# Kernel tuning notes

Hardware: AMD Instinct MI355X
Metric: run time of the kernel (lower is better)

Reference implementation:

```python
import jax, jax.numpy as jnp
import numpy as np
from functools import partial

L, E, H, FF = 6, 768, 12, 3072
D = E // H
EPS = 1e-5

def _layernorm(x, g, b):
    mu = jnp.mean(x, axis=-1, keepdims=True)
    var = jnp.mean(jnp.square(x - mu), axis=-1, keepdims=True)
    return (x - mu) * jax.lax.rsqrt(var + EPS) * g + b

def setup_inputs() -> dict:
    key = jax.random.key(0)
    ks = jax.random.split(key, 16)
    s = 0.02
    return {
        "inputs_embeds": jax.random.normal(ks[0], (2, 1024, E), jnp.float32),
        "attention_mask": jnp.ones((2, 1024), jnp.float32),
        "Wqkv": jax.random.normal(ks[1], (L, E, 3 * E), jnp.float32) * s,
        "bqkv": jnp.zeros((L, 3 * E), jnp.float32),
        "Wo": jax.random.normal(ks[2], (L, E, E), jnp.float32) * s,
        "bo": jnp.zeros((L, E), jnp.float32),
        "ln1_g": jnp.ones((L, E), jnp.float32),
        "ln1_b": jnp.zeros((L, E), jnp.float32),
        "ln2_g": jnp.ones((L, E), jnp.float32),
        "ln2_b": jnp.zeros((L, E), jnp.float32),
        "Wfc": jax.random.normal(ks[3], (L, E, FF), jnp.float32) * s,
        "bfc": jnp.zeros((L, FF), jnp.float32),
        "Wmo": jax.random.normal(ks[4], (L, FF, E), jnp.float32) * s,
        "bmo": jnp.zeros((L, E), jnp.float32),
        "lnf_g": jnp.ones((E,), jnp.float32),
        "lnf_b": jnp.zeros((E,), jnp.float32),
    }

def reference(inputs_embeds, attention_mask, Wqkv, bqkv, Wo, bo,
              ln1_g, ln1_b, ln2_g, ln2_b, Wfc, bfc, Wmo, bmo, lnf_g, lnf_b):
    B, S, _ = inputs_embeds.shape
    # additive mask, broadcast over heads and query positions: [B,1,1,S]
    mask_add = (1.0 - attention_mask)[:, None, None, :] * -10000.0
    scale = 1.0 / jnp.sqrt(jnp.float32(D))

    def block(x, p):
        wqkv, bq, wo_, bo_, g1, b1, g2, b2, wfc, bf, wmo, bm = p
        h = _layernorm(x, g1, b1)
        qkv = h @ wqkv + bq                      # [B,S,3E]
        q, k, v = jnp.split(qkv, 3, axis=-1)
        q = q.reshape(B, S, H, D).transpose(0, 2, 1, 3)  # [B,H,S,D]
        k = k.reshape(B, S, H, D).transpose(0, 2, 1, 3)
        v = v.reshape(B, S, H, D).transpose(0, 2, 1, 3)
        scores = jnp.einsum('bhqd,bhkd->bhqk', q, k) * scale + mask_add
        w = jax.nn.softmax(scores, axis=-1)
        a = jnp.einsum('bhqk,bhkd->bhqd', w, v)
        a = a.transpose(0, 2, 1, 3).reshape(B, S, E)
        x = x + a @ wo_ + bo_
        m = _layernorm(x, g2, b2)
        m = jax.nn.gelu(m @ wfc + bf, approximate=False) @ wmo + bm
        x = x + m
        return x, None

    params = (Wqkv, bqkv, Wo, bo, ln1_g, ln1_b, ln2_g, ln2_b, Wfc, bfc, Wmo, bmo)
    x, _ = jax.lax.scan(block, inputs_embeds, params)
    return _layernorm(x, lnf_g, lnf_b)
```

## Files before the change

kernel.cpp:

```cpp
#include <hip/hip_runtime.h>
#include <hip/hip_bf16.h>
#include <math.h>

constexpr int LYR = 6;
constexpr int E   = 768;
constexpr int NH  = 12;
constexpr int FFD = 3072;
constexpr int HD  = 64;
constexpr int BB  = 2;
constexpr int SS  = 1024;
constexpr int T   = BB * SS;
constexpr int E3  = 3 * E;
constexpr int FH  = FFD / 2;

constexpr size_t SZ_QKV_T = (size_t)E3 * E;
constexpr size_t SZ_WO_T  = (size_t)E * E;
constexpr size_t SZ_WFC_T = (size_t)FFD * E;
constexpr size_t SZ_WMO_T = (size_t)E * FFD;
constexpr size_t LSZ      = SZ_QKV_T + SZ_WO_T + SZ_WFC_T + SZ_WMO_T;
constexpr int TQ = (E3 / 32) * (E / 32);
constexpr int TO = (E / 32) * (E / 32);
constexpr int TF = (FFD / 32) * (E / 32);
constexpr int TM = (E / 32) * (FFD / 32);
constexpr int TL = TQ + TO + TF + TM;

#define LN_EPS 1e-5f

typedef __attribute__((ext_vector_type(8))) short    short8v;
typedef __attribute__((ext_vector_type(8))) unsigned short ushort8v;
typedef __attribute__((ext_vector_type(4))) unsigned short ushort4v;
typedef __attribute__((ext_vector_type(4))) float    f32x4;

__device__ __forceinline__ float bf2f(__hip_bfloat16 x) { return __bfloat162float(x); }
__device__ __forceinline__ float bfr2f(unsigned short u) {
    union { unsigned int i; float f; } v; v.i = ((unsigned int)u) << 16; return v.f;
}
__device__ __forceinline__ __hip_bfloat16 f2bf(float f) { return __float2bfloat16(f); }
__device__ __forceinline__ unsigned short f2bfbits(float f) {
    union { float f; unsigned int i; } v; v.f = f;
    unsigned int r = (v.i + 0x7fffu + ((v.i >> 16) & 1u)) >> 16;
    return (unsigned short)r;
}

__device__ __forceinline__ float block_sum(float v, float* sm) {
    #pragma unroll
    for (int o = 32; o > 0; o >>= 1) v += __shfl_down(v, o, 64);
    int lane = threadIdx.x & 63, wid = threadIdx.x >> 6;
    if (lane == 0) sm[wid] = v;
    __syncthreads();
    float r = sm[0] + sm[1] + sm[2] + sm[3];
    __syncthreads();
    return r;
}

__device__ __forceinline__ float block_max(float v, float* sm) {
    #pragma unroll
    for (int o = 32; o > 0; o >>= 1) v = fmaxf(v, __shfl_down(v, o, 64));
    int lane = threadIdx.x & 63, wid = threadIdx.x >> 6;
    if (lane == 0) sm[wid] = v;
    __syncthreads();
    float r = fmaxf(fmaxf(sm[0], sm[1]), fmaxf(sm[2], sm[3]));
    __syncthreads();
    return r;
}

__global__ void copy4_kernel(const float4* __restrict__ in, float4* __restrict__ out, int n4) {
    int i = blockIdx.x * 256 + threadIdx.x;
    if (i < n4) out[i] = in[i];
}

__global__ void rowstat_kernel(const float* __restrict__ x, float2* __restrict__ musig) {
    __shared__ float sm[4];
    int row = blockIdx.x;
    const float* xr = x + (size_t)row * E;
    float s = 0.f;
    for (int i = threadIdx.x; i < E; i += 256) s += xr[i];
    float mu = block_sum(s, sm) * (1.0f / E);
    float v = 0.f;
    for (int i = threadIdx.x; i < E; i += 256) { float d = xr[i] - mu; v += d * d; }
    float rstd = rsqrtf(block_sum(v, sm) * (1.0f / E) + LN_EPS);
    if (threadIdx.x == 0) musig[row] = make_float2(mu, rstd);
}

template <typename OT>
__global__ void ln_kernel(const float* __restrict__ x, OT* __restrict__ out,
                          const float* __restrict__ g, const float* __restrict__ b) {
    __shared__ float sm[4];
    int row = blockIdx.x;
    const float* xr = x + (size_t)row * E;
    float s = 0.f;
    for (int i = threadIdx.x; i < E; i += 256) s += xr[i];
    float mu = block_sum(s, sm) * (1.0f / E);
    float v = 0.f;
    for (int i = threadIdx.x; i < E; i += 256) { float d = xr[i] - mu; v += d * d; }
    float rstd = rsqrtf(block_sum(v, sm) * (1.0f / E) + LN_EPS);
    for (int i = threadIdx.x; i < E; i += 256) {
        float o = (xr[i] - mu) * rstd * g[i] + b[i];
        if constexpr (sizeof(OT) == 2) out[(size_t)row * E + i] = f2bf(o);
        else                           out[(size_t)row * E + i] = o;
    }
}

__device__ __forceinline__ void transpose_tile(const float* __restrict__ W,
                                               unsigned short* __restrict__ Wt,
                                               int K, int N, int n0, int k0) {
    __shared__ float tile[32][33];
    int tx = threadIdx.x & 31, ty = threadIdx.x >> 5;
    #pragma unroll
    for (int i = 0; i < 4; i++)
        tile[ty + i * 8][tx] = W[(size_t)(k0 + ty + i * 8) * N + n0 + tx];
    __syncthreads();
    #pragma unroll
    for (int i = 0; i < 4; i++)
        Wt[(size_t)(n0 + ty + i * 8) * K + k0 + tx] = f2bfbits(tile[tx][ty + i * 8]);
}

__global__ void transpose_cvt(const float* __restrict__ W, unsigned short* __restrict__ Wt,
                              int K, int N) {
    transpose_tile(W, Wt, K, N, blockIdx.x * 32, blockIdx.y * 32);
}

__global__ void transpose_all(const float* __restrict__ Wqkv, const float* __restrict__ Wo,
                              const float* __restrict__ Wfc, const float* __restrict__ Wmo,
                              unsigned short* __restrict__ wt_all) {
    int bid = blockIdx.x;
    int layer = bid / TL, lid = bid % TL;
    unsigned short* dst = wt_all + (size_t)layer * LSZ;
    const float* W; int K, N, t;
    if (lid < TQ)                { W = Wqkv + (size_t)layer * E * E3;  K = E;   N = E3;  t = lid; }
    else if (lid < TQ + TO)      { W = Wo   + (size_t)layer * E * E;   K = E;   N = E;   t = lid - TQ;
                                   dst += SZ_QKV_T; }
    else if (lid < TQ + TO + TF) { W = Wfc  + (size_t)layer * E * FFD; K = E;   N = FFD; t = lid - TQ - TO;
                                   dst += SZ_QKV_T + SZ_WO_T; }
    else                         { W = Wmo  + (size_t)layer * FFD * E; K = FFD; N = E;   t = lid - TQ - TO - TF;
                                   dst += SZ_QKV_T + SZ_WO_T + SZ_WFC_T; }
    int nt = N / 32;
    transpose_tile(W, dst, K, N, (t % nt) * 32, (t / nt) * 32);
}

template <int FUSE>
__global__ __launch_bounds__(512) void gemm_bt(
        const unsigned short* __restrict__ A, int lda,
        const unsigned short* __restrict__ Bt, int ldb,
        const float* __restrict__ bias,
        void* __restrict__ Cptr, int ldc, int K) {
    constexpr int BM = 64, BN = 128, PAD = 80;
    constexpr int MFR = 2, NFR = 2;
    __shared__ unsigned short As[BM * PAD];
    __shared__ unsigned short Bs[BN * PAD];

    int tid = threadIdx.x;
    int bm = blockIdx.y * BM, bn = blockIdx.x * BN;
    int kchunk = K / gridDim.z;
    int kbeg = blockIdx.z * kchunk, kend = kbeg + kchunk;
    int w = tid >> 6, lane = tid & 63, ln16 = lane & 15, q = lane >> 4;
    int wm = (w & 1) * 32, wn = (w >> 1) * 32;

    f32x4 acc[MFR][NFR];
    #pragma unroll
    for (int i = 0; i < MFR; i++)
        #pragma unroll
        for (int j = 0; j < NFR; j++) acc[i][j] = (f32x4){0.f, 0.f, 0.f, 0.f};

    for (int k0 = kbeg; k0 < kend; k0 += 64) {
        {
            int row = tid >> 3, ko = (tid & 7) * 8;
            *(ushort8v*)(&As[row * PAD + ko]) =
                *(const ushort8v*)(A + (size_t)(bm + row) * lda + k0 + ko);
        }
        #pragma unroll
        for (int i = 0; i < 2; i++) {
            int idx = tid + i * 512;
            int row = idx >> 3, ko = (idx & 7) * 8;
            *(ushort8v*)(&Bs[row * PAD + ko]) =
                *(const ushort8v*)(Bt + (size_t)(bn + row) * ldb + k0 + ko);
        }
        __syncthreads();

        #pragma unroll
        for (int kk = 0; kk < 64; kk += 32) {
            short8v afr[MFR], bfr[NFR];
            #pragma unroll
            for (int i = 0; i < MFR; i++)
                afr[i] = *(const short8v*)(&As[(wm + i * 16 + ln16) * PAD + kk + q * 8]);
            #pragma unroll
            for (int j = 0; j < NFR; j++)
                bfr[j] = *(const short8v*)(&Bs[(wn + j * 16 + ln16) * PAD + kk + q * 8]);
            #pragma unroll
            for (int i = 0; i < MFR; i++)
                #pragma unroll
                for (int j = 0; j < NFR; j++)
                    acc[i][j] = __builtin_amdgcn_mfma_f32_16x16x32_bf16(afr[i], bfr[j], acc[i][j], 0, 0, 0);
        }
        __syncthreads();
    }

    #pragma unroll
    for (int j = 0; j < NFR; j++) {
        int col = bn + wn + j * 16 + ln16;
        float bv = (blockIdx.z == 0) ? bias[col] : 0.f;
        #pragma unroll
        for (int i = 0; i < MFR; i++) {
            #pragma unroll
            for (int r = 0; r < 4; r++) {
                int row = bm + wm + i * 16 + q * 4 + r;
                float v = acc[i][j][r] + bv;
                if (FUSE == 1) v = 0.5f * v * (1.0f + erff(v * 0.70710678118654752f));
                if (FUSE == 0 || FUSE == 1) {
                    ((unsigned short*)Cptr)[(size_t)row * ldc + col] = f2bfbits(v);
                } else {
                    atomicAdd(&((float*)Cptr)[(size_t)row * ldc + col], v);
                }
            }
        }
    }
}

__global__ __launch_bounds__(128) void attn_mfma(unsigned short* __restrict__ qkv,
                                                 const float* __restrict__ mask) {
    constexpr int KP = 80;
    constexpr int VP = 80;
    constexpr int PP = 82;
    __shared__ unsigned short Ks[64 * KP];
    __shared__ unsigned short Vt[64 * VP];
    __shared__ unsigned short Ps[32 * PP];
    __shared__ float Ms[64];

    int bid = blockIdx.x;
    int qt = bid & 31;
    int h  = (bid >> 5) % NH;
    int b  = bid / (32 * NH);
    int tid = threadIdx.x;
    int w = tid >> 6, lane = tid & 63, ln16 = lane & 15, q4 = lane >> 4;

    int qrow = b * SS + qt * 32 + w * 16 + ln16;
    const unsigned short* qbase = qkv + (size_t)qrow * E3 + h * HD;
    short8v qfr0 = *(const short8v*)(qbase + q4 * 8);
    short8v qfr1 = *(const short8v*)(qbase + 32 + q4 * 8);

    f32x4 sacc[4];
    f32x4 oacc[4];
    float m_run[4], l_run[4];
    #pragma unroll
    for (int r = 0; r < 4; r++) { m_run[r] = -1e30f; l_run[r] = 0.f; }
    #pragma unroll
    for (int i = 0; i < 4; i++) oacc[i] = (f32x4){0.f, 0.f, 0.f, 0.f};

    for (int t = 0; t < 16; t++) {
        int j0 = t * 64;
        #pragma unroll
        for (int i = 0; i < 4; i++) {
            int idx = tid + i * 128;
            int row = idx >> 3, ko = (idx & 7) * 8;
            size_t gb = (size_t)(b * SS + j0 + row) * E3 + h * HD;
            *(ushort8v*)(&Ks[row * KP + ko]) = *(const ushort8v*)(qkv + gb + E + ko);
        }
        #pragma unroll
        for (int i = 0; i < 4; i++) {
            int ko = (w + 2 * i) * 8;
            size_t gb = (size_t)(b * SS + j0 + lane) * E3 + h * HD + 2 * E + ko;
            ushort8v vv = *(const ushort8v*)(qkv + gb);
            #pragma unroll
            for (int e = 0; e < 8; e++)
                Vt[(ko + e) * VP + lane] = vv[e];
        }
        if (tid < 64) Ms[tid] = (1.0f - mask[b * SS + j0 + tid]) * -10000.0f;
        __syncthreads();

        #pragma unroll
        for (int jf = 0; jf < 4; jf++) sacc[jf] = (f32x4){0.f, 0.f, 0.f, 0.f};
        #pragma unroll
        for (int jf = 0; jf < 4; jf++) {
            short8v k0f = *(const short8v*)(&Ks[(jf * 16 + ln16) * KP + q4 * 8]);
            short8v k1f = *(const short8v*)(&Ks[(jf * 16 + ln16) * KP + 32 + q4 * 8]);
            sacc[jf] = __builtin_amdgcn_mfma_f32_16x16x32_bf16(qfr0, k0f, sacc[jf], 0, 0, 0);
            sacc[jf] = __builtin_amdgcn_mfma_f32_16x16x32_bf16(qfr1, k1f, sacc[jf], 0, 0, 0);
        }

        float madd[4];
        #pragma unroll
        for (int jf = 0; jf < 4; jf++) madd[jf] = Ms[jf * 16 + ln16];
        #pragma unroll
        for (int jf = 0; jf < 4; jf++)
            #pragma unroll
            for (int r = 0; r < 4; r++)
                sacc[jf][r] = sacc[jf][r] * 0.125f + madd[jf];

        #pragma unroll
        for (int r = 0; r < 4; r++) {
            float mx = fmaxf(fmaxf(sacc[0][r], sacc[1][r]), fmaxf(sacc[2][r], sacc[3][r]));
            mx = fmaxf(mx, __shfl_xor(mx, 1, 64));
            mx = fmaxf(mx, __shfl_xor(mx, 2, 64));
            mx = fmaxf(mx, __shfl_xor(mx, 4, 64));
            mx = fmaxf(mx, __shfl_xor(mx, 8, 64));
            float mnew = fmaxf(m_run[r], mx);
            float alpha = __expf(m_run[r] - mnew);
            m_run[r] = mnew;
            float ps = 0.f;
            #pragma unroll
            for (int jf = 0; jf < 4; jf++) {
                float p = __expf(sacc[jf][r] - mnew);
                sacc[jf][r] = p;
                ps += p;
            }
            ps += __shfl_xor(ps, 1, 64);
            ps += __shfl_xor(ps, 2, 64);
            ps += __shfl_xor(ps, 4, 64);
            ps += __shfl_xor(ps, 8, 64);
            l_run[r] = l_run[r] * alpha + ps;
            #pragma unroll
            for (int df = 0; df < 4; df++) oacc[df][r] *= alpha;
        }

        #pragma unroll
        for (int jf = 0; jf < 4; jf++)
            #pragma unroll
            for (int r = 0; r < 4; r++)
                Ps[(w * 16 + q4 * 4 + r) * PP + jf * 16 + ln16] = f2bfbits(sacc[jf][r]);

        short8v pa0 = *(const short8v*)(&Ps[(w * 16 + ln16) * PP + q4 * 8]);
        short8v pa1 = *(const short8v*)(&Ps[(w * 16 + ln16) * PP + 32 + q4 * 8]);
        #pragma unroll
        for (int df = 0; df < 4; df++) {
            short8v v0f = *(const short8v*)(&Vt[(df * 16 + ln16) * VP + q4 * 8]);
            short8v v1f = *(const short8v*)(&Vt[(df * 16 + ln16) * VP + 32 + q4 * 8]);
            oacc[df] = __builtin_amdgcn_mfma_f32_16x16x32_bf16(pa0, v0f, oacc[df], 0, 0, 0);
            oacc[df] = __builtin_amdgcn_mfma_f32_16x16x32_bf16(pa1, v1f, oacc[df], 0, 0, 0);
        }
        __syncthreads();
    }

    #pragma unroll
    for (int r = 0; r < 4; r++) {
        float inv = 1.0f / l_run[r];
        int row = b * SS + qt * 32 + w * 16 + q4 * 4 + r;
        size_t ob = (size_t)row * E3 + h * HD;
        #pragma unroll
        for (int df = 0; df < 4; df++)
            qkv[ob + df * 16 + ln16] = f2bfbits(oacc[df][r] * inv);
    }
}

template <int AMODE, int FUSE>
__global__ void gemm_mfma(const void* __restrict__ Aptr, int lda,
                          const float* __restrict__ W, int ldw,
                          const float* __restrict__ bias,
                          const float2* __restrict__ musig,
                          const float* __restrict__ lng, const float* __restrict__ lnb,
                          void* __restrict__ Cptr, int ldc, int K) {
    __shared__ unsigned short As[128 * 40];
    __shared__ unsigned short Bs[32 * 130];

    int tid = threadIdx.x;
    int bm = blockIdx.y * 128, bn = blockIdx.x * 128;
    int w = tid >> 6, lane = tid & 63, ln16 = lane & 15, q = lane >> 4;
    int wm = (w & 1) * 64, wn = (w >> 1) * 64;

    f32x4 acc[4][4];
    #pragma unroll
    for (int i = 0; i < 4; i++)
        #pragma unroll
        for (int j = 0; j < 4; j++) acc[i][j] = (f32x4){0.f, 0.f, 0.f, 0.f};

    for (int k0 = 0; k0 < K; k0 += 32) {
        if (AMODE == 0) {
            const unsigned short* A = (const unsigned short*)Aptr;
            #pragma unroll
            for (int i = 0; i < 2; i++) {
                int idx = tid + i * 256;
                int row = idx >> 2, ko = (idx & 3) * 8;
                ushort8v v = *(const ushort8v*)(A + (size_t)(bm + row) * lda + k0 + ko);
                *(ushort8v*)(&As[row * 40 + ko]) = v;
            }
        } else {
            const float* A = (const float*)Aptr;
            #pragma unroll
            for (int i = 0; i < 4; i++) {
                int idx = tid + i * 256;
                int row = idx >> 3, ko = (idx & 7) * 4;
                float4 xv = *(const float4*)(A + (size_t)(bm + row) * lda + k0 + ko);
                float2 ms = musig[bm + row];
                float4 gv = *(const float4*)(lng + k0 + ko);
                float4 bv = *(const float4*)(lnb + k0 + ko);
                ushort4v o;
                o[0] = f2bfbits((xv.x - ms.x) * ms.y * gv.x + bv.x);
                o[1] = f2bfbits((xv.y - ms.x) * ms.y * gv.y + bv.y);
                o[2] = f2bfbits((xv.z - ms.x) * ms.y * gv.z + bv.z);
                o[3] = f2bfbits((xv.w - ms.x) * ms.y * gv.w + bv.w);
                *(ushort4v*)(&As[row * 40 + ko]) = o;
            }
        }
        #pragma unroll
        for (int i = 0; i < 16; i++) {
            int idx = tid + i * 256;
            int kr = idx >> 7, n = idx & 127;
            float wv = W[(size_t)(k0 + kr) * ldw + bn + n];
            Bs[kr * 130 + n] = f2bfbits(wv);
        }
        __syncthreads();

        short8v afr[4], bfr[4];
        #pragma unroll
        for (int i = 0; i < 4; i++)
            afr[i] = *(const short8v*)(&As[(wm + i * 16 + ln16) * 40 + q * 8]);
        #pragma unroll
        for (int j = 0; j < 4; j++) {
            int n = wn + j * 16 + ln16;
            #pragma unroll
            for (int jj = 0; jj < 8; jj++)
                bfr[j][jj] = (short)Bs[(q * 8 + jj) * 130 + n];
        }
        #pragma unroll
        for (int i = 0; i < 4; i++)
            #pragma unroll
            for (int j = 0; j < 4; j++)
                acc[i][j] = __builtin_amdgcn_mfma_f32_16x16x32_bf16(afr[i], bfr[j], acc[i][j], 0, 0, 0);
        __syncthreads();
    }

    #pragma unroll
    for (int j = 0; j < 4; j++) {
        int col = bn + wn + j * 16 + ln16;
        float bv = (FUSE == 3) ? 0.f : bias[col];
        #pragma unroll
        for (int i = 0; i < 4; i++) {
            #pragma unroll
            for (int r = 0; r < 4; r++) {
                int row = bm + wm + i * 16 + q * 4 + r;
                float v = acc[i][j][r] + bv;
                if (FUSE == 1) v = 0.5f * v * (1.0f + erff(v * 0.70710678118654752f));
                if (FUSE == 0 || FUSE == 1) {
                    ((unsigned short*)Cptr)[(size_t)row * ldc + col] = f2bfbits(v);
                } else {
                    float* C = (float*)Cptr;
                    C[(size_t)row * ldc + col] += v;
                }
            }
        }
    }
}

__global__ void attn_flash(unsigned short* __restrict__ qkv,
                           const float* __restrict__ mask) {
    __shared__ float Qs[32][68];
    __shared__ float Ks[64][68];
    __shared__ float Vs[64][68];
    __shared__ float Ps[32][68];

    int bid = blockIdx.x;
    int qt = bid & 31;
    int h  = (bid >> 5) % NH;
    int b  = bid / (32 * NH);
    int tid = threadIdx.x;
    int ql = tid >> 3, grp = tid & 7;

    #pragma unroll
    for (int i = 0; i < 8; i++) {
        int idx = tid + i * 256;
        int rq = idx >> 6, d = idx & 63;
        int grow = b * SS + qt * 32 + rq;
        Qs[rq][d] = bfr2f(qkv[(size_t)grow * E3 + h * HD + d]) * 0.125f;
    }

    float m_run = -1e30f, l_run = 0.f;
    float O[8] = {0.f, 0.f, 0.f, 0.f, 0.f, 0.f, 0.f, 0.f};

    for (int c = 0; c < 16; c++) {
        int j0 = c * 64;
        #pragma unroll
        for (int i = 0; i < 4; i++) {
            int idx = tid + i * 256;
            int jj = idx >> 4, d4 = (idx & 15) * 4;
            size_t base = (size_t)(b * SS + j0 + jj) * E3 + h * HD + d4;
            ushort4v kv = *(const ushort4v*)(qkv + base + E);
            ushort4v vv = *(const ushort4v*)(qkv + base + 2 * E);
            *(float4*)&Ks[jj][d4] = make_float4(bfr2f(kv[0]), bfr2f(kv[1]), bfr2f(kv[2]), bfr2f(kv[3]));
            *(float4*)&Vs[jj][d4] = make_float4(bfr2f(vv[0]), bfr2f(vv[1]), bfr2f(vv[2]), bfr2f(vv[3]));
        }
        __syncthreads();

        float s[8] = {0.f, 0.f, 0.f, 0.f, 0.f, 0.f, 0.f, 0.f};
        #pragma unroll
        for (int d0 = 0; d0 < 64; d0 += 4) {
            float4 q4 = *(const float4*)&Qs[ql][d0];
            #pragma unroll
            for (int jl = 0; jl < 8; jl++) {
                float4 k4 = *(const float4*)&Ks[grp + jl * 8][d0];
                s[jl] += q4.x * k4.x + q4.y * k4.y + q4.z * k4.z + q4.w * k4.w;
            }
        }
        #pragma unroll
        for (int jl = 0; jl < 8; jl++)
            s[jl] += (1.0f - mask[b * SS + j0 + grp + jl * 8]) * -10000.0f;

        float cm = s[0];
        #pragma unroll
        for (int jl = 1; jl < 8; jl++) cm = fmaxf(cm, s[jl]);
        cm = fmaxf(cm, __shfl_xor(cm, 1, 64));
        cm = fmaxf(cm, __shfl_xor(cm, 2, 64));
        cm = fmaxf(cm, __shfl_xor(cm, 4, 64));

        float mnew = fmaxf(m_run, cm);
        float alpha = __expf(m_run - mnew);
        float ps = 0.f;
        #pragma unroll
        for (int jl = 0; jl < 8; jl++) {
            float p = __expf(s[jl] - mnew);
            Ps[ql][grp + jl * 8] = p;
            ps += p;
        }
        ps += __shfl_xor(ps, 1, 64);
        ps += __shfl_xor(ps, 2, 64);
        ps += __shfl_xor(ps, 4, 64);
        l_run = l_run * alpha + ps;
        m_run = mnew;
        #pragma unroll
        for (int e = 0; e < 8; e++) O[e] *= alpha;

        #pragma unroll 4
        for (int jj = 0; jj < 64; jj++) {
            float p = Ps[ql][jj];
            float4 v0 = *(const float4*)&Vs[jj][grp * 8];
            float4 v1 = *(const float4*)&Vs[jj][grp * 8 + 4];
            O[0] += p * v0.x; O[1] += p * v0.y; O[2] += p * v0.z; O[3] += p * v0.w;
            O[4] += p * v1.x; O[5] += p * v1.y; O[6] += p * v1.z; O[7] += p * v1.w;
        }
        __syncthreads();
    }

    float inv = 1.0f / l_run;
    int grow = b * SS + qt * 32 + ql;
    size_t obase = (size_t)grow * E3 + h * HD + grp * 8;
    #pragma unroll
    for (int e = 0; e < 8; e++)
        qkv[obase + e] = f2bfbits(O[e] * inv);
}

template <int FUSE, typename CT>
__global__ void gemm_legacy(const __hip_bfloat16* __restrict__ A, int lda,
                            const float* __restrict__ W, int ldw,
                            const float* __restrict__ bias,
                            CT* __restrict__ C, int ldc,
                            const float* __restrict__ resid,
                            int M, int N, int K) {
    __shared__ float As[16][65];
    __shared__ float Bs[16][65];
    int bm = blockIdx.y * 64, bn = blockIdx.x * 64;
    int tid = threadIdx.x;
    int ty = tid >> 4, tx = tid & 15;
    int ar = tid >> 2, ak = (tid & 3) << 2;
    int wk = tid >> 4, wn = (tid & 15) << 2;

    float acc[4][4] = {};
    for (int k0 = 0; k0 < K; k0 += 16) {
        ushort4 av = *(const ushort4*)(A + (size_t)(bm + ar) * lda + k0 + ak);
        As[ak + 0][ar] = bfr2f(av.x);
        As[ak + 1][ar] = bfr2f(av.y);
        As[ak + 2][ar] = bfr2f(av.z);
        As[ak + 3][ar] = bfr2f(av.w);
        float4 wv = *(const float4*)(W + (size_t)(k0 + wk) * ldw + bn + wn);
        Bs[wk][wn + 0] = wv.x;
        Bs[wk][wn + 1] = wv.y;
        Bs[wk][wn + 2] = wv.z;
        Bs[wk][wn + 3] = wv.w;
        __syncthreads();
        #pragma unroll
        for (int kk = 0; kk < 16; kk++) {
            float a[4], bv[4];
            #pragma unroll
            for (int i = 0; i < 4; i++) { a[i] = As[kk][ty * 4 + i]; bv[i] = Bs[kk][tx * 4 + i]; }
            #pragma unroll
            for (int i = 0; i < 4; i++)
                #pragma unroll
                for (int j = 0; j < 4; j++) acc[i][j] += a[i] * bv[j];
        }
        __syncthreads();
    }
    #pragma unroll
    for (int i = 0; i < 4; i++) {
        int row = bm + ty * 4 + i;
        #pragma unroll
        for (int j = 0; j < 4; j++) {
            int col = bn + tx * 4 + j;
            float v = acc[i][j];
            if (FUSE != 3) v += bias[col];
            if (FUSE == 1) v = 0.5f * v * (1.0f + erff(v * 0.70710678118654752f));
            if (FUSE == 2 || FUSE == 3) v += resid[(size_t)row * ldc + col];
            if constexpr (sizeof(CT) == 2) C[(size_t)row * ldc + col] = f2bf(v);
            else                           C[(size_t)row * ldc + col] = v;
        }
    }
}

__global__ void attn_legacy(const __hip_bfloat16* __restrict__ qkv,
                            const float* __restrict__ mask,
                            __hip_bfloat16* __restrict__ out) {
    __shared__ float sc[SS];
    __shared__ float qv[HD];
    __shared__ float oacc[4][HD];
    __shared__ float redbuf[4];

    int q = blockIdx.x & (SS - 1);
    int h = blockIdx.x >> 10;
    int tid = threadIdx.x;

    const __hip_bfloat16* qrow = qkv + (size_t)q * E3 + h * HD;
    if (tid < HD) qv[tid] = bf2f(qrow[tid]) * 0.125f;
    __syncthreads();

    for (int j = tid; j < SS; j += 256) {
        const __hip_bfloat16* krow = qkv + (size_t)j * E3 + E + h * HD;
        float d = 0.f;
        #pragma unroll
        for (int t = 0; t < HD; t += 4) {
            ushort4 kv4 = *(const ushort4*)(krow + t);
            d += qv[t] * bfr2f(kv4.x) + qv[t + 1] * bfr2f(kv4.y)
               + qv[t + 2] * bfr2f(kv4.z) + qv[t + 3] * bfr2f(kv4.w);
        }
        d += (1.0f - mask[j]) * -10000.0f;
        sc[j] = d;
    }
    __syncthreads();

    float m = -1e30f;
    for (int j = tid; j < SS; j += 256) m = fmaxf(m, sc[j]);
    m = block_max(m, redbuf);
    float s = 0.f;
    for (int j = tid; j < SS; j += 256) { float e = __expf(sc[j] - m); sc[j] = e; s += e; }
    s = block_sum(s, redbuf);
    float inv = 1.0f / s;
    __syncthreads();

    int d = tid & 63, c = tid >> 6;
    float acc = 0.f;
    int j0 = c * 256;
    for (int j = j0; j < j0 + 256; j++) {
        const __hip_bfloat16* vrow = qkv + (size_t)j * E3 + 2 * E + h * HD;
        acc += sc[j] * bf2f(vrow[d]);
    }
    oacc[c][d] = acc;
    __syncthreads();
    if (tid < HD) {
        float o = (oacc[0][tid] + oacc[1][tid] + oacc[2][tid] + oacc[3][tid]) * inv;
        out[(size_t)q * E + h * HD + tid] = f2bf(o);
    }
}

__global__ void copy_kernel(const float* __restrict__ in, float* __restrict__ out, int n) {
    int i = blockIdx.x * 256 + threadIdx.x;
    if (i < n) out[i] = in[i];
}

extern "C" void kernel_launch(void* const* d_in, const int* in_sizes, int n_in,
                              void* d_out, int out_size, void* d_ws, size_t ws_size,
                              hipStream_t stream) {
    const float* emb   = (const float*)d_in[0];
    const float* mask  = (const float*)d_in[1];
    const float* Wqkv  = (const float*)d_in[2];
    const float* bqkv  = (const float*)d_in[3];
    const float* Wo    = (const float*)d_in[4];
    const float* bo    = (const float*)d_in[5];
    const float* ln1g  = (const float*)d_in[6];
    const float* ln1b  = (const float*)d_in[7];
    const float* ln2g  = (const float*)d_in[8];
    const float* ln2b  = (const float*)d_in[9];
    const float* Wfc   = (const float*)d_in[10];
    const float* bfc   = (const float*)d_in[11];
    const float* Wmo   = (const float*)d_in[12];
    const float* bmo   = (const float*)d_in[13];
    const float* lnfg  = (const float*)d_in[14];
    const float* lnfb  = (const float*)d_in[15];

    const size_t NEED_FAST3 = sizeof(float) * (size_t)T * E
                            + 2ull * (size_t)T * E
                            + 2ull * (size_t)T * FFD
                            + 2ull * 6 * LSZ;
    const size_t NEED_FAST2 = sizeof(float) * (size_t)T * E
                            + 2ull * (size_t)T * E
                            + 2ull * (size_t)T * FFD
                            + 2ull * (size_t)E * FFD;
    const size_t NEED_FAST = sizeof(float) * (size_t)T * E
                           + 2ull * (size_t)T * E3
                           + sizeof(float2) * (size_t)T;

    if (ws_size >= NEED_FAST2) {
        const bool allw = (ws_size >= NEED_FAST3);
        float* x            = (float*)d_ws;
        unsigned short* h   = (unsigned short*)(x + (size_t)T * E);
        unsigned short* buf = h + (size_t)T * E;
        unsigned short* wt  = buf + (size_t)T * FFD;
        unsigned short* qkv = buf;
        unsigned short* ff  = buf;

        copy4_kernel<<<dim3(T * E / 4 / 256), dim3(256), 0, stream>>>(
            (const float4*)emb, (float4*)x, T * E / 4);

        if (allw) {
            transpose_all<<<dim3(6 * TL), dim3(256), 0, stream>>>(Wqkv, Wo, Wfc, Wmo, wt);
        }

        for (int l = 0; l < LYR; l++) {
            const float* wqkv_l = Wqkv + (size_t)l * E * E3;
            const float* wo_l   = Wo   + (size_t)l * E * E;
            const float* wfc_l  = Wfc  + (size_t)l * E * FFD;
            const float* wmo_l  = Wmo  + (size_t)l * FFD * E;

            const unsigned short* wq_t, *wo_t, *wfc_t, *wmo_t;
            if (allw) {
                const unsigned short* base = wt + (size_t)l * LSZ;
                wq_t  = base;
                wo_t  = base + SZ_QKV_T;
                wfc_t = base + SZ_QKV_T + SZ_WO_T;
                wmo_t = base + SZ_QKV_T + SZ_WO_T + SZ_WFC_T;
            } else {
                wq_t = wo_t = wfc_t = wmo_t = wt;
            }

            ln_kernel<__hip_bfloat16><<<dim3(T), dim3(256), 0, stream>>>(
                x, (__hip_bfloat16*)h, ln1g + l * E, ln1b + l * E);
            if (!allw)
                transpose_cvt<<<dim3(E3 / 32, E / 32), dim3(256), 0, stream>>>(wqkv_l, wt, E, E3);
            gemm_bt<0><<<dim3(E3 / 128, T / 64), dim3(512), 0, stream>>>(
                h, E, wq_t, E, bqkv + l * E3, qkv, E3, E);
            attn_mfma<<<dim3(BB * NH * 32), dim3(128), 0, stream>>>(qkv, mask);
            if (!allw)
                transpose_cvt<<<dim3(E / 32, E / 32), dim3(256), 0, stream>>>(wo_l, wt, E, E);
            gemm_bt<2><<<dim3(E / 128, T / 64, 4), dim3(512), 0, stream>>>(
                qkv, E3, wo_t, E, bo + l * E, x, E, E);

            ln_kernel<__hip_bfloat16><<<dim3(T), dim3(256), 0, stream>>>(
                x, (__hip_bfloat16*)h, ln2g + l * E, ln2b + l * E);
            if (!allw)
                transpose_cvt<<<dim3(FFD / 32, E / 32), dim3(256), 0, stream>>>(wfc_l, wt, E, FFD);
            gemm_bt<1><<<dim3(FFD / 128, T / 64), dim3(512), 0, stream>>>(
                h, E, wfc_t, E, bfc + l * FFD, ff, FFD, E);
            if (!allw)
                transpose_cvt<<<dim3(E / 32, FFD / 32), dim3(256), 0, stream>>>(wmo_l, wt, FFD, E);
            gemm_bt<2><<<dim3(E / 128, T / 64, 4), dim3(512), 0, stream>>>(
                ff, FFD, wmo_t, FFD, bmo + l * E, x, E, FFD);
        }
        ln_kernel<float><<<dim3(T), dim3(256), 0, stream>>>(x, (float*)d_out, lnfg, lnfb);
    } else if (ws_size >= NEED_FAST) {
        float* x              = (float*)d_ws;
        unsigned short* qkv   = (unsigned short*)(x + (size_t)T * E);
        float2* musig         = (float2*)(qkv + (size_t)T * E3);

        copy4_kernel<<<dim3(T * E / 4 / 256), dim3(256), 0, stream>>>(
            (const float4*)emb, (float4*)x, T * E / 4);

        for (int l = 0; l < LYR; l++) {
            const float* wqkv_l = Wqkv + (size_t)l * E * E3;
            const float* wo_l   = Wo   + (size_t)l * E * E;
            const float* wfc_l  = Wfc  + (size_t)l * E * FFD;
            const float* wmo_l  = Wmo  + (size_t)l * FFD * E;

            rowstat_kernel<<<dim3(T), dim3(256), 0, stream>>>(x, musig);
            gemm_mfma<1, 0><<<dim3(E3 / 128, T / 128), dim3(256), 0, stream>>>(
                x, E, wqkv_l, E3, bqkv + l * E3, musig, ln1g + l * E, ln1b + l * E,
                qkv, E3, E);
            attn_flash<<<dim3(BB * NH * 32), dim3(256), 0, stream>>>(qkv, mask);
            gemm_mfma<0, 2><<<dim3(E / 128, T / 128), dim3(256), 0, stream>>>(
                qkv, E3, wo_l, E, bo + l * E, nullptr, nullptr, nullptr, x, E, E);

            unsigned short* ffp = qkv;
            unsigned short* hp  = qkv + (size_t)T * FH;
            ln_kernel<__hip_bfloat16><<<dim3(T), dim3(256), 0, stream>>>(
                x, (__hip_bfloat16*)hp, ln2g + l * E, ln2b + l * E);
            for (int f = 0; f < 2; f++) {
                gemm_mfma<0, 1><<<dim3(FH / 128, T / 128), dim3(256), 0, stream>>>(
                    hp, E, wfc_l + f * FH, FFD, bfc + l * FFD + f * FH,
                    nullptr, nullptr, nullptr, ffp, FH, E);
                if (f == 0)
                    gemm_mfma<0, 3><<<dim3(E / 128, T / 128), dim3(256), 0, stream>>>(
                        ffp, FH, wmo_l + (size_t)f * FH * E, E, nullptr, nullptr, nullptr, nullptr,
                        x, E, FH);
                else
                    gemm_mfma<0, 2><<<dim3(E / 128, T / 128), dim3(256), 0, stream>>>(
                        ffp, FH, wmo_l + (size_t)f * FH * E, E, bmo + l * E, nullptr, nullptr, nullptr,
                        x, E, FH);
            }
        }
        ln_kernel<float><<<dim3(T), dim3(256), 0, stream>>>(x, (float*)d_out, lnfg, lnfb);
    } else {
        float* x           = (float*)d_ws;
        __hip_bfloat16* hb = (__hip_bfloat16*)(x + (size_t)T * E);
        __hip_bfloat16* qb = hb + (size_t)SS * E;

        int n = T * E;
        copy_kernel<<<dim3((n + 255) / 256), dim3(256), 0, stream>>>(emb, x, n);

        for (int l = 0; l < LYR; l++) {
            const float* wqkv_l = Wqkv + (size_t)l * E * E3;
            const float* wo_l   = Wo   + (size_t)l * E * E;
            const float* wfc_l  = Wfc  + (size_t)l * E * FFD;
            const float* wmo_l  = Wmo  + (size_t)l * FFD * E;

            for (int b = 0; b < BB; b++) {
                float* xb = x + (size_t)b * SS * E;
                ln_kernel<__hip_bfloat16><<<dim3(SS), dim3(256), 0, stream>>>(
                    xb, hb, ln1g + l * E, ln1b + l * E);
                gemm_legacy<0, __hip_bfloat16><<<dim3(E3 / 64, SS / 64), dim3(256), 0, stream>>>(
                    hb, E, wqkv_l, E3, bqkv + l * E3, qb, E3, nullptr, SS, E3, E);
                attn_legacy<<<dim3(NH * SS), dim3(256), 0, stream>>>(qb, mask + b * SS, hb);
                gemm_legacy<2, float><<<dim3(E / 64, SS / 64), dim3(256), 0, stream>>>(
                    hb, E, wo_l, E, bo + l * E, xb, E, xb, SS, E, E);
            }
            for (int b = 0; b < BB; b++) {
                float* xb = x + (size_t)b * SS * E;
                ln_kernel<__hip_bfloat16><<<dim3(SS), dim3(256), 0, stream>>>(
                    xb, hb, ln2g + l * E, ln2b + l * E);
                for (int f = 0; f < 2; f++) {
                    gemm_legacy<1, __hip_bfloat16><<<dim3(FH / 64, SS / 64), dim3(256), 0, stream>>>(
                        hb, E, wfc_l + f * FH, FFD, bfc + l * FFD + f * FH, qb, FH, nullptr,
                        SS, FH, E);
                    if (f == 0)
                        gemm_legacy<3, float><<<dim3(E / 64, SS / 64), dim3(256), 0, stream>>>(
                            qb, FH, wmo_l + (size_t)f * FH * E, E, nullptr, xb, E, xb, SS, E, FH);
                    else
                        gemm_legacy<2, float><<<dim3(E / 64, SS / 64), dim3(256), 0, stream>>>(
                            qb, FH, wmo_l + (size_t)f * FH * E, E, bmo + l * E, xb, E, xb, SS, E, FH);
                }
            }
        }
        ln_kernel<float><<<dim3(T), dim3(256), 0, stream>>>(x, (float*)d_out, lnfg, lnfb);
    }
}
```

Before: 1.110 ms.

## Prefetch GEMM and attention tiles into registers, widen weight transpose, raise split-K

The bf16 GEMM now loads the next K-tile from global memory into registers while the MFMA work on the current tile runs. The attention kernel double-buffers its K/V/mask shared-memory tiles with register prefetch, so loads overlap compute and one barrier per iteration is removed. The one-time weight transpose uses 64x64 tiles with float4 reads and 8-wide bf16 writes. The MLP down-projection split-K factor rises from 4 to 6, adding more atomics in exchange for more blocks. Register pressure and shared memory use go up.

```diff
diff --git a/kernel.cpp b/kernel.cpp
--- a/kernel.cpp
+++ b/kernel.cpp
@@ -18,10 +18,10 @@
 constexpr size_t SZ_WFC_T = (size_t)FFD * E;
 constexpr size_t SZ_WMO_T = (size_t)E * FFD;
 constexpr size_t LSZ      = SZ_QKV_T + SZ_WO_T + SZ_WFC_T + SZ_WMO_T;
-constexpr int TQ = (E3 / 32) * (E / 32);
-constexpr int TO = (E / 32) * (E / 32);
-constexpr int TF = (FFD / 32) * (E / 32);
-constexpr int TM = (E / 32) * (FFD / 32);
+constexpr int TQ = (E3 / 64) * (E / 64);
+constexpr int TO = (E / 64) * (E / 64);
+constexpr int TF = (FFD / 64) * (E / 64);
+constexpr int TM = (E / 64) * (FFD / 64);
 constexpr int TL = TQ + TO + TF + TM;
 
 #define LN_EPS 1e-5f
@@ -120,6 +120,32 @@
     transpose_tile(W, Wt, K, N, blockIdx.x * 32, blockIdx.y * 32);
 }
 
+__device__ __forceinline__ void transpose_tile64(const float* __restrict__ W,
+                                                 unsigned short* __restrict__ Wt,
+                                                 int K, int N, int n0, int k0) {
+    __shared__ float tile[64][65];
+    int tid = threadIdx.x;
+    int rr = tid >> 4, c4 = (tid & 15) * 4;
+    #pragma unroll
+    for (int i = 0; i < 4; i++) {
+        float4 v = *(const float4*)&W[(size_t)(k0 + rr + i * 16) * N + n0 + c4];
+        tile[rr + i * 16][c4 + 0] = v.x;
+        tile[rr + i * 16][c4 + 1] = v.y;
+        tile[rr + i * 16][c4 + 2] = v.z;
+        tile[rr + i * 16][c4 + 3] = v.w;
+    }
+    __syncthreads();
+    int nr = tid >> 3, kc = (tid & 7) * 8;
+    #pragma unroll
+    for (int i = 0; i < 2; i++) {
+        int n = nr + i * 32;
+        ushort8v o;
+        #pragma unroll
+        for (int e = 0; e < 8; e++) o[e] = f2bfbits(tile[kc + e][n]);
+        *(ushort8v*)&Wt[(size_t)(n0 + n) * K + k0 + kc] = o;
+    }
+}
+
 __global__ void transpose_all(const float* __restrict__ Wqkv, const float* __restrict__ Wo,
                               const float* __restrict__ Wfc, const float* __restrict__ Wmo,
                               unsigned short* __restrict__ wt_all) {
@@ -134,8 +160,8 @@
                                    dst += SZ_QKV_T + SZ_WO_T; }
     else                         { W = Wmo  + (size_t)layer * FFD * E; K = FFD; N = E;   t = lid - TQ - TO - TF;
                                    dst += SZ_QKV_T + SZ_WO_T + SZ_WFC_T; }
-    int nt = N / 32;
-    transpose_tile(W, dst, K, N, (t % nt) * 32, (t / nt) * 32);
+    int nt = N / 64;
+    transpose_tile64(W, dst, K, N, (t % nt) * 64, (t / nt) * 64);
 }
 
 template <int FUSE>
@@ -156,26 +182,32 @@
     int w = tid >> 6, lane = tid & 63, ln16 = lane & 15, q = lane >> 4;
     int wm = (w & 1) * 32, wn = (w >> 1) * 32;
 
+    int rowA = tid >> 3, koA = (tid & 7) * 8;
+    int rowB0 = tid >> 3, koB = (tid & 7) * 8;
+    int rowB1 = (tid + 512) >> 3;
+
     f32x4 acc[MFR][NFR];
     #pragma unroll
     for (int i = 0; i < MFR; i++)
         #pragma unroll
         for (int j = 0; j < NFR; j++) acc[i][j] = (f32x4){0.f, 0.f, 0.f, 0.f};
 
+    ushort8v aR, bR0, bR1;
+    aR  = *(const ushort8v*)(A  + (size_t)(bm + rowA)  * lda + kbeg + koA);
+    bR0 = *(const ushort8v*)(Bt + (size_t)(bn + rowB0) * ldb + kbeg + koB);
+    bR1 = *(const ushort8v*)(Bt + (size_t)(bn + rowB1) * ldb + kbeg + koB);
+
     for (int k0 = kbeg; k0 < kend; k0 += 64) {
-        {
-            int row = tid >> 3, ko = (tid & 7) * 8;
-            *(ushort8v*)(&As[row * PAD + ko]) =
-                *(const ushort8v*)(A + (size_t)(bm + row) * lda + k0 + ko);
-        }
-        #pragma unroll
-        for (int i = 0; i < 2; i++) {
-            int idx = tid + i * 512;
-            int row = idx >> 3, ko = (idx & 7) * 8;
-            *(ushort8v*)(&Bs[row * PAD + ko]) =
-                *(const ushort8v*)(Bt + (size_t)(bn + row) * ldb + k0 + ko);
-        }
+        *(ushort8v*)(&As[rowA * PAD + koA])  = aR;
+        *(ushort8v*)(&Bs[rowB0 * PAD + koB]) = bR0;
+        *(ushort8v*)(&Bs[rowB1 * PAD + koB]) = bR1;
         __syncthreads();
+
+        if (k0 + 64 < kend) {
+            aR  = *(const ushort8v*)(A  + (size_t)(bm + rowA)  * lda + k0 + 64 + koA);
+            bR0 = *(const ushort8v*)(Bt + (size_t)(bn + rowB0) * ldb + k0 + 64 + koB);
+            bR1 = *(const ushort8v*)(Bt + (size_t)(bn + rowB1) * ldb + k0 + 64 + koB);
+        }
 
         #pragma unroll
         for (int kk = 0; kk < 64; kk += 32) {
@@ -221,10 +253,10 @@
     constexpr int KP = 80;
     constexpr int VP = 80;
     constexpr int PP = 82;
-    __shared__ unsigned short Ks[64 * KP];
-    __shared__ unsigned short Vt[64 * VP];
+    __shared__ unsigned short Ks[2][64 * KP];
+    __shared__ unsigned short Vt[2][64 * VP];
     __shared__ unsigned short Ps[32 * PP];
-    __shared__ float Ms[64];
+    __shared__ float Ms[2][64];
 
     int bid = blockIdx.x;
     int qt = bid & 31;
@@ -238,6 +270,9 @@
     short8v qfr0 = *(const short8v*)(qbase + q4 * 8);
     short8v qfr1 = *(const short8v*)(qbase + 32 + q4 * 8);
 
+    ushort8v kR[4], vR[4];
+    float mR = 1.0f;
+
     f32x4 sacc[4];
     f32x4 oacc[4];
     float m_run[4], l_run[4];
@@ -246,40 +281,65 @@
     #pragma unroll
     for (int i = 0; i < 4; i++) oacc[i] = (f32x4){0.f, 0.f, 0.f, 0.f};
 
-    for (int t = 0; t < 16; t++) {
-        int j0 = t * 64;
+    {
+        int j0 = 0;
         #pragma unroll
         for (int i = 0; i < 4; i++) {
-            int idx = tid + i * 128;
-            int row = idx >> 3, ko = (idx & 7) * 8;
-            size_t gb = (size_t)(b * SS + j0 + row) * E3 + h * HD;
-            *(ushort8v*)(&Ks[row * KP + ko]) = *(const ushort8v*)(qkv + gb + E + ko);
+            int idx = tid + i * 128; int row = idx >> 3, ko = (idx & 7) * 8;
+            kR[i] = *(const ushort8v*)(qkv + (size_t)(b * SS + j0 + row) * E3 + h * HD + E + ko);
         }
         #pragma unroll
         for (int i = 0; i < 4; i++) {
             int ko = (w + 2 * i) * 8;
-            size_t gb = (size_t)(b * SS + j0 + lane) * E3 + h * HD + 2 * E + ko;
-            ushort8v vv = *(const ushort8v*)(qkv + gb);
+            vR[i] = *(const ushort8v*)(qkv + (size_t)(b * SS + j0 + lane) * E3 + h * HD + 2 * E + ko);
+        }
+        if (tid < 64) mR = mask[b * SS + j0 + tid];
+        #pragma unroll
+        for (int i = 0; i < 4; i++) {
+            int idx = tid + i * 128; int row = idx >> 3, ko = (idx & 7) * 8;
+            *(ushort8v*)(&Ks[0][row * KP + ko]) = kR[i];
+        }
+        #pragma unroll
+        for (int i = 0; i < 4; i++) {
+            int ko = (w + 2 * i) * 8;
             #pragma unroll
             for (int e = 0; e < 8; e++)
-                Vt[(ko + e) * VP + lane] = vv[e];
-        }
-        if (tid < 64) Ms[tid] = (1.0f - mask[b * SS + j0 + tid]) * -10000.0f;
-        __syncthreads();
+                Vt[0][(ko + e) * VP + lane] = vR[i][e];
+        }
+        if (tid < 64) Ms[0][tid] = (1.0f - mR) * -10000.0f;
+    }
+    __syncthreads();
+
+    for (int t = 0; t < 16; t++) {
+        int cur = t & 1;
+        if (t < 15) {
+            int j0 = (t + 1) * 64;
+            #pragma unroll
+            for (int i = 0; i < 4; i++) {
+                int idx = tid + i * 128; int row = idx >> 3, ko = (idx & 7) * 8;
+                kR[i] = *(const ushort8v*)(qkv + (size_t)(b * SS + j0 + row) * E3 + h * HD + E + ko);
+            }
+            #pragma unroll
+            for (int i = 0; i < 4; i++) {
+                int ko = (w + 2 * i) * 8;
+                vR[i] = *(const ushort8v*)(qkv + (size_t)(b * SS + j0 + lane) * E3 + h * HD + 2 * E + ko);
+            }
+            if (tid < 64) mR = mask[b * SS + j0 + tid];
+        }
 
         #pragma unroll
         for (int jf = 0; jf < 4; jf++) sacc[jf] = (f32x4){0.f, 0.f, 0.f, 0.f};
         #pragma unroll
         for (int jf = 0; jf < 4; jf++) {
-            short8v k0f = *(const short8v*)(&Ks[(jf * 16 + ln16) * KP + q4 * 8]);
-            short8v k1f = *(const short8v*)(&Ks[(jf * 16 + ln16) * KP + 32 + q4 * 8]);
+            short8v k0f = *(const short8v*)(&Ks[cur][(jf * 16 + ln16) * KP + q4 * 8]);
+            short8v k1f = *(const short8v*)(&Ks[cur][(jf * 16 + ln16) * KP + 32 + q4 * 8]);
             sacc[jf] = __builtin_amdgcn_mfma_f32_16x16x32_bf16(qfr0, k0f, sacc[jf], 0, 0, 0);
             sacc[jf] = __builtin_amdgcn_mfma_f32_16x16x32_bf16(qfr1, k1f, sacc[jf], 0, 0, 0);
         }
 
         float madd[4];
         #pragma unroll
-        for (int jf = 0; jf < 4; jf++) madd[jf] = Ms[jf * 16 + ln16];
+        for (int jf = 0; jf < 4; jf++) madd[jf] = Ms[cur][jf * 16 + ln16];
         #pragma unroll
         for (int jf = 0; jf < 4; jf++)
             #pragma unroll
@@ -322,10 +382,27 @@
         short8v pa1 = *(const short8v*)(&Ps[(w * 16 + ln16) * PP + 32 + q4 * 8]);
         #pragma unroll
         for (int df = 0; df < 4; df++) {
-            short8v v0f = *(const short8v*)(&Vt[(df * 16 + ln16) * VP + q4 * 8]);
-            short8v v1f = *(const short8v*)(&Vt[(df * 16 + ln16) * VP + 32 + q4 * 8]);
+            short8v v0f = *(const short8v*)(&Vt[cur][(df * 16 + ln16) * VP + q4 * 8]);
+            short8v v1f = *(const short8v*)(&Vt[cur][(df * 16 + ln16) * VP + 32 + q4 * 8]);
             oacc[df] = __builtin_amdgcn_mfma_f32_16x16x32_bf16(pa0, v0f, oacc[df], 0, 0, 0);
             oacc[df] = __builtin_amdgcn_mfma_f32_16x16x32_bf16(pa1, v1f, oacc[df], 0, 0, 0);
+        }
+
+        if (t < 15) {
+            int nb = cur ^ 1;
+            #pragma unroll
+            for (int i = 0; i < 4; i++) {
+                int idx = tid + i * 128; int row = idx >> 3, ko = (idx & 7) * 8;
+                *(ushort8v*)(&Ks[nb][row * KP + ko]) = kR[i];
+            }
+            #pragma unroll
+            for (int i = 0; i < 4; i++) {
+                int ko = (w + 2 * i) * 8;
+                #pragma unroll
+                for (int e = 0; e < 8; e++)
+                    Vt[nb][(ko + e) * VP + lane] = vR[i][e];
+            }
+            if (tid < 64) Ms[nb][tid] = (1.0f - mR) * -10000.0f;
         }
         __syncthreads();
     }
@@ -736,7 +813,7 @@
                 h, E, wfc_t, E, bfc + l * FFD, ff, FFD, E);
             if (!allw)
                 transpose_cvt<<<dim3(E / 32, FFD / 32), dim3(256), 0, stream>>>(wmo_l, wt, FFD, E);
-            gemm_bt<2><<<dim3(E / 128, T / 64, 4), dim3(512), 0, stream>>>(
+            gemm_bt<2><<<dim3(E / 128, T / 64, 6), dim3(512), 0, stream>>>(
                 ff, FFD, wmo_t, FFD, bmo + l * E, x, E, FFD);
         }
         ln_kernel<float><<<dim3(T), dim3(256), 0, stream>>>(x, (float*)d_out, lnfg, lnfb);
```

Result: no change. 1.092 ms (-1.6%).
